# Optimization experiments

Hardware: AMD Instinct MI355X
Metric: run time of the kernel (lower is better)

## Reference

```python
import jax, jax.numpy as jnp
import numpy as np

ANG = 7
N = ANG * ANG          # 49 views
CENTER = N // 2        # index 24 = central view
EDGE_C = 150.0
ALPHA = 0.1
CROP = 8
GAUSS = jnp.array([[0.0751, 0.1238, 0.0751],
                   [0.1238, 0.2042, 0.1238],
                   [0.0751, 0.1238, 0.0751]], dtype=jnp.float32)


def _edge_aware_smoothness(D, I):
    # D: [b,h,w] disparity; I: [b,3,h,w] center view
    gx = I[:, :, :, 1:] - I[:, :, :, :-1]
    gy = I[:, :, 1:, :] - I[:, :, :-1, :]
    wx = jnp.exp(-EDGE_C * jnp.mean(jnp.abs(gx), axis=1, keepdims=True))
    wy = jnp.exp(-EDGE_C * jnp.mean(jnp.abs(gy), axis=1, keepdims=True))
    Du = D[:, None]
    dgx = Du[:, :, :, 1:] - Du[:, :, :, :-1]
    dgy = Du[:, :, 1:, :] - Du[:, :, :-1, :]
    lx = jnp.mean((wx * jnp.abs(dgx))[:, :, CROP:-CROP, CROP:-CROP])
    ly = jnp.mean((wy * jnp.abs(dgy))[:, :, CROP:-CROP, CROP:-CROP])
    return (lx + ly) / 2.0


def _warp_all(pred, x):
    # Backward-warp each of the 49 views toward the center view using the
    # per-pixel disparity scaled by the view's angular offset (bilinear,
    # border-clamped) -- standard light-field warping (warp_all in the repo).
    # pred: [b,h,w]; x: [b,3,N,h,w] -> warped [b,3,N,h,w]
    b, c, n, h, w = x.shape
    off = jnp.arange(ANG, dtype=pred.dtype) - (ANG // 2)
    du = jnp.repeat(off, ANG)   # row (u) offset per view, [N]
    dv = jnp.tile(off, ANG)     # col (v) offset per view, [N]
    gy = jnp.arange(h, dtype=pred.dtype)[:, None]
    gx = jnp.arange(w, dtype=pred.dtype)[None, :]
    p = pred[:, None, :, :]                                # [b,1,h,w]
    cy = jnp.clip(gy[None, None] + p * du[None, :, None, None], 0.0, h - 1)
    cx = jnp.clip(gx[None, None] + p * dv[None, :, None, None], 0.0, w - 1)
    y0f = jnp.floor(cy); x0f = jnp.floor(cx)
    ty = (cy - y0f)[..., None]; tx = (cx - x0f)[..., None]
    y0 = y0f.astype(jnp.int32); x0 = x0f.astype(jnp.int32)
    y1 = jnp.minimum(y0 + 1, h - 1); x1 = jnp.minimum(x0 + 1, w - 1)
    img = jnp.transpose(x, (0, 2, 3, 4, 1)).reshape(b, n, h * w, c)

    def gather(yi, xi):
        idx = (yi * w + xi).reshape(b, n, h * w, 1)
        return jnp.take_along_axis(img, idx, axis=2).reshape(b, n, h, w, c)

    out = (gather(y0, x0) * (1 - ty) * (1 - tx)
           + gather(y0, x1) * (1 - ty) * tx
           + gather(y1, x0) * ty * (1 - tx)
           + gather(y1, x1) * ty * tx)
    return jnp.transpose(out, (0, 4, 1, 2, 3))


def _gauss_smooth_angular(cl):
    # cl [b,1,N,h,w]: 3x3 gaussian conv over the 7x7 angular grid, replicate pad
    b, _, _, h, w = cl.shape
    g = cl.reshape(b, 1, ANG, ANG, h, w)
    g = jnp.pad(g, ((0, 0), (0, 0), (1, 1), (1, 1), (0, 0), (0, 0)), mode='edge')
    out = sum(GAUSS[i, j] * g[:, :, i:i + ANG, j:j + ANG]
              for i in range(3) for j in range(3))
    return out.reshape(b, 1, N, h, w)


def _forward(pred, x, y, epoch):
    b, u, v, h, w, c = x.shape
    # 'b u v h w c -> b c (u v) h w'
    xr = jnp.transpose(x, (0, 5, 1, 2, 3, 4)).reshape(b, c, N, h, w)
    center = xr[:, :, CENTER]                               # [b,3,h,w]
    grad_loss = _edge_aware_smoothness(pred, center)
    warped = _warp_all(pred, xr)                            # [b,3,N,h,w]
    color_loss = jnp.mean(jnp.abs(warped - warped[:, :, CENTER:CENTER + 1]),
                          axis=1, keepdims=True)            # [b,1,N,h,w]
    if epoch > 0:
        gauss = jax.lax.stop_gradient(_gauss_smooth_angular(color_loss))
        idx = jnp.argsort(-gauss, axis=2)                   # descending
        sorted_cl = jnp.take_along_axis(color_loss, idx, axis=2)
    else:
        sorted_cl = -jnp.sort(-color_loss, axis=2)
    yb = y[:, None, None, :, :]
    ar = jnp.arange(N, dtype=y.dtype)[None, None, :, None, None]
    mask = (ar > yb).astype(color_loss.dtype) / (N - yb) * N
    if epoch > 0:
        mask = jax.lax.stop_gradient(mask)                  # torch no_grad branch
    cl = jnp.mean((sorted_cl * mask)[..., CROP:-CROP, CROP:-CROP])
    return cl + grad_loss * ALPHA


def setup_inputs():
    key = jax.random.key(0)
    k1, k2, k3 = jax.random.split(key, 3)
    b, h, w = 4, 256, 256
    pred = jax.random.normal(k1, (b, h, w), dtype=jnp.float32)
    x = jax.random.uniform(k2, (b, ANG, ANG, h, w, 3), dtype=jnp.float32)
    y = jax.random.uniform(k3, (b, h, w), dtype=jnp.float32) * 24.0  # keep ~half views
    return {"pred": pred, "x": x, "y": y, "epoch": 5}


def reference(pred, x, y, epoch):
    return _forward(pred, x, y, epoch)
```

## Files before the change

### kernel.cpp

```cpp
#include <hip/hip_runtime.h>
#include <math.h>

#define NV    49
#define NVP   52
#define Himg  256
#define Wimg  256
#define RW    240
#define RWH   (RW*RW)
#define NPIX  (4*RWH)
#define ROWF  (Wimg*3)
#define IMGF  (Himg*Wimg*3)
#define NBLK  (NPIX/64)

typedef float f4u __attribute__((ext_vector_type(4), aligned(4)));
typedef float f2u __attribute__((ext_vector_type(2), aligned(4)));
typedef float f4a __attribute__((ext_vector_type(4), aligned(16)));


__global__ __launch_bounds__(448, 4) void color_kernel(
    const float* __restrict__ pred, const float* __restrict__ x,
    const float* __restrict__ y, const int* __restrict__ epoch_p,
    double* __restrict__ acc)
{
    __shared__ float s_cl[64 * NVP];
    __shared__ float s_g [64 * NVP];
    __shared__ float sred[8];

    const int tid = threadIdx.x;
    const int pix = tid & 63;
    const int sub = __builtin_amdgcn_readfirstlane(tid >> 6);

    int lb  = (blockIdx.x & 7) * (NBLK/8) + (blockIdx.x >> 3);
    int pid = lb * 64 + pix;
    int b   = pid / RWH;
    int rem = pid - b * RWH;
    int ry  = rem / RW;
    int yy  = 8 + ry;
    int xx  = 8 + (rem - ry * RW);

    int pidx = (b * Himg + yy) * Wimg + xx;
    float p    = pred[pidx];
    float yval = y[pidx];
    const int epoch = *epoch_p;

    const float* xv    = x + (size_t)b * (49 * IMGF);
    const float* cbase = xv + (24 * IMGF) + (yy * Wimg + xx) * 3;
    f4u cv = *(const f4u*)cbase;
    float c0 = cv.x, c1 = cv.y, c2 = cv.z;

    float* mycl = s_cl + pix * NVP;
    float* myg  = s_g  + pix * NVP;

    int co[7]; float txv[7];
    #pragma unroll
    for (int vv = 0; vv < 7; vv++) {
        float cx = fminf(fmaxf((float)xx + p * (float)(vv-3), 0.0f), 255.0f);
        float x0f = floorf(cx);
        float tx = cx - x0f;
        int ix0 = (int)x0f;
        if (ix0 >= 255) { ix0 = 254; tx = 1.0f; }
        co[vv] = ix0 * 3; txv[vv] = tx;
    }

    float creg[7];
    {
        float cy = fminf(fmaxf((float)yy + p * (float)(sub-3), 0.0f), 255.0f);
        float y0f = floorf(cy);
        float ty = cy - y0f;
        int iy0 = (int)y0f;
        int iy1 = min(iy0+1, 255);
        int ro0 = iy0*ROWF, ro1 = iy1*ROWF;
        const float* vbase = xv + sub * 7 * IMGF;

        f4u a0[4], b0[4]; f2u a1[4], b1[4];

#define LOADV(VV, S) { \
        const float* s0p = vbase + (VV)*IMGF + ro0 + co[VV]; \
        const float* s1p = vbase + (VV)*IMGF + ro1 + co[VV]; \
        a0[S] = *(const f4u*)s0p;  a1[S] = *(const f2u*)(s0p + 4); \
        b0[S] = *(const f4u*)s1p;  b1[S] = *(const f2u*)(s1p + 4); }

        LOADV(0,0) LOADV(1,1) LOADV(2,2)
        __builtin_amdgcn_sched_barrier(0);

        #pragma unroll
        for (int vv = 0; vv < 7; vv++) {
            if (vv + 3 < 7) { LOADV(vv+3, (vv+3)&3) }
            __builtin_amdgcn_sched_barrier(0);
            const int S = vv & 3;
            float tx = txv[vv];
            float s00 = a0[S].x, s01 = a0[S].y, s02 = a0[S].z;
            float s03 = a0[S].w, s04 = a1[S].x, s05 = a1[S].y;
            float s10 = b0[S].x, s11 = b0[S].y, s12 = b0[S].z;
            float s13 = b0[S].w, s14 = b1[S].x, s15 = b1[S].y;
            float h0 = s00 + tx*(s03-s00);
            float h1 = s01 + tx*(s04-s01);
            float h2 = s02 + tx*(s05-s02);
            float k0 = s10 + tx*(s13-s10);
            float k1 = s11 + tx*(s14-s11);
            float k2 = s12 + tx*(s15-s12);
            float o0 = h0 + ty*(k0-h0);
            float o1 = h1 + ty*(k1-h1);
            float o2 = h2 + ty*(k2-h2);
            float cl = (fabsf(o0-c0)+fabsf(o1-c1)+fabsf(o2-c2)) * (1.0f/3.0f);
            creg[vv] = cl;
            mycl[sub*7 + vv] = cl;
            __builtin_amdgcn_sched_barrier(0);
        }
#undef LOADV
    }

    if (sub == 3) {
        float lx = 0.0f, ly = 0.0f;
        if (xx <= 246) {
            f4u q0 = *(const f4u*)cbase;
            f2u q1 = *(const f2u*)(cbase + 4);
            float wx = __expf(-50.0f * (fabsf(q0.w-c0) + fabsf(q1.x-c1) + fabsf(q1.y-c2)));
            lx = wx * fabsf(pred[pidx + 1] - p);
        }
        if (yy <= 246) {
            f4u r = *(const f4u*)(cbase + ROWF);
            float wy = __expf(-50.0f * (fabsf(r.x-c0) + fabsf(r.y-c1) + fabsf(r.z-c2)));
            ly = wy * fabsf(pred[pidx + Wimg] - p);
        }
        #pragma unroll
        for (int off = 32; off > 0; off >>= 1) {
            lx += __shfl_down(lx, off);
            ly += __shfl_down(ly, off);
        }
        if (pix == 0) {
            atomicAdd(acc + 1, (double)lx);
            atomicAdd(acc + 2, (double)ly);
        }
    }
    __syncthreads();

    if (epoch > 0) {
        const int um1 = (sub > 0) ? sub-1 : 0;
        const int up1 = (sub < 6) ? sub+1 : 6;
        const float* rm = mycl + um1*7;
        const float* rc = mycl + sub*7;
        const float* rp = mycl + up1*7;
        #pragma unroll
        for (int vv = 0; vv < 7; vv++) {
            const int vm = (vv > 0) ? vv-1 : 0;
            const int vp = (vv < 6) ? vv+1 : 6;
            myg[sub*7 + vv] =
                0.0751f*rm[vm] + 0.1238f*rm[vv] + 0.0751f*rm[vp] +
                0.1238f*rc[vm] + 0.2042f*rc[vv] + 0.1238f*rc[vp] +
                0.0751f*rp[vm] + 0.1238f*rp[vv] + 0.0751f*rp[vp];
        }
    }
    __syncthreads();

    const float* keyb = (epoch > 0) ? myg : mycl;

    f4a kv[13];
    #pragma unroll
    for (int i = 0; i < 13; i++)
        kv[i] = *(const f4a*)(keyb + 4*i);

    unsigned long long kn[7];
    int cnt[7];
    #pragma unroll
    for (int i = 0; i < 7; i++) {
        int n = sub*7 + i;
        unsigned int bb = __float_as_uint(keyb[n]);
        kn[i] = (((unsigned long long)bb) << 8) | (unsigned long long)(255 - n);
        cnt[i] = 0;
    }
    #pragma unroll
    for (int m = 0; m < NV; m++) {
        unsigned int bm = __float_as_uint(kv[m>>2][m&3]);
        unsigned long long km = (((unsigned long long)bm) << 8) | (unsigned long long)(255 - m);
        #pragma unroll
        for (int i = 0; i < 7; i++)
            cnt[i] += (km > kn[i]) ? 1 : 0;
    }
    float tail = 0.0f;
    #pragma unroll
    for (int i = 0; i < 7; i++)
        tail += ((float)cnt[i] > yval) ? creg[i] : 0.0f;
    float contrib = tail * (49.0f / (49.0f - yval));

    #pragma unroll
    for (int off = 32; off > 0; off >>= 1)
        contrib += __shfl_down(contrib, off);
    if (pix == 0) sred[sub] = contrib;
    __syncthreads();
    if (tid == 0) {
        double s = 0.0;
        #pragma unroll
        for (int i = 0; i < 7; i++) s += (double)sred[i];
        atomicAdd(acc + 0, s);
    }
}

__global__ void finalize_kernel(const double* __restrict__ acc,
                                float* __restrict__ out)
{
    double cl = acc[0] / 11289600.0;
    double gl = (acc[1] + acc[2]) / (2.0 * 229440.0);
    out[0] = (float)(cl + 0.1 * gl);
}

extern "C" void kernel_launch(void* const* d_in, const int* in_sizes, int n_in,
                              void* d_out, int out_size, void* d_ws, size_t ws_size,
                              hipStream_t stream)
{
    const float* pred  = (const float*)d_in[0];
    const float* x     = (const float*)d_in[1];
    const float* y     = (const float*)d_in[2];
    const int*   epoch = (const int*)d_in[3];
    double* acc = (double*)d_ws;

    hipMemsetAsync(acc, 0, 3 * sizeof(double), stream);
    color_kernel<<<NBLK, 448, 0, stream>>>(pred, x, y, epoch, acc);
    finalize_kernel<<<1, 1, 0, stream>>>(acc, (float*)d_out);
}
```

Baseline: 320.3 us.

## Split fused color kernel into per-view cl kernel and per-pixel rank kernel

Replaces the single fused kernel with two passes. The first computes the per-view color loss with one thread per pixel and view, plus the smoothness term, and writes it to a workspace buffer. The second loads all 49 values per pixel into registers, does the angular Gaussian smoothing and rank counting, and accumulates the result. This removes the shared-memory exchange and the sync stalls, and gives a more regular gather pattern per view. In exchange it adds about 45 MB of intermediate writes and reads and heavy register pressure in the rank kernel. The old kernel is kept as a fallback when the workspace is too small.

New measurement: 497.9 us. +55.4%, slower.

```diff
diff --git a/kernel.cpp b/kernel.cpp
--- a/kernel.cpp
+++ b/kernel.cpp
@@ -15,6 +15,152 @@
 typedef float f4u __attribute__((ext_vector_type(4), aligned(4)));
 typedef float f2u __attribute__((ext_vector_type(2), aligned(4)));
 typedef float f4a __attribute__((ext_vector_type(4), aligned(16)));
+
+
+__global__ __launch_bounds__(256) void cl_kernel(
+    const float* __restrict__ pred, const float* __restrict__ x,
+    float* __restrict__ clbuf, double* __restrict__ acc)
+{
+    const int tid = threadIdx.x;
+    const int nb  = blockIdx.y;
+    const int b   = nb & 3;
+    const int n   = nb >> 2;
+    const int u   = n / 7, v = n - u*7;
+
+    int pix = blockIdx.x*256 + tid;
+    int ry  = pix / RW;
+    int rx  = pix - ry*RW;
+    int yy  = 8 + ry, xx = 8 + rx;
+    int pidx = (b*Himg + yy)*Wimg + xx;
+    float p = pred[pidx];
+
+    const float* xv    = x + (size_t)b * (49*IMGF);
+    const float* cbase = xv + 24*IMGF + (yy*Wimg+xx)*3;
+    f4u cv = *(const f4u*)cbase;
+    float c0 = cv.x, c1 = cv.y, c2 = cv.z;
+
+    float cx  = fminf(fmaxf((float)xx + p*(float)(v-3), 0.0f), 255.0f);
+    float x0f = floorf(cx);
+    float tx  = cx - x0f;
+    int ix0   = (int)x0f;
+    if (ix0 >= 255) { ix0 = 254; tx = 1.0f; }
+    float cy  = fminf(fmaxf((float)yy + p*(float)(u-3), 0.0f), 255.0f);
+    float y0f = floorf(cy);
+    float ty  = cy - y0f;
+    int iy0   = (int)y0f;
+    int iy1   = min(iy0+1, 255);
+
+    const float* ib  = xv + n*IMGF;
+    const float* s0p = ib + iy0*ROWF + ix0*3;
+    const float* s1p = ib + iy1*ROWF + ix0*3;
+    f4u a0 = *(const f4u*)s0p;  f2u a1 = *(const f2u*)(s0p + 4);
+    f4u b0 = *(const f4u*)s1p;  f2u b1 = *(const f2u*)(s1p + 4);
+
+    float s00 = a0.x, s01 = a0.y, s02 = a0.z;
+    float s03 = a0.w, s04 = a1.x, s05 = a1.y;
+    float s10 = b0.x, s11 = b0.y, s12 = b0.z;
+    float s13 = b0.w, s14 = b1.x, s15 = b1.y;
+    float h0 = s00 + tx*(s03-s00);
+    float h1 = s01 + tx*(s04-s01);
+    float h2 = s02 + tx*(s05-s02);
+    float k0 = s10 + tx*(s13-s10);
+    float k1 = s11 + tx*(s14-s11);
+    float k2 = s12 + tx*(s15-s12);
+    float o0 = h0 + ty*(k0-h0);
+    float o1 = h1 + ty*(k1-h1);
+    float o2 = h2 + ty*(k2-h2);
+    float cl = (fabsf(o0-c0)+fabsf(o1-c1)+fabsf(o2-c2)) * (1.0f/3.0f);
+
+    clbuf[(size_t)nb*RWH + pix] = cl;
+
+    if (n == 24) {
+        float lx = 0.0f, ly = 0.0f;
+        if (xx <= 246) {
+            f2u q1 = *(const f2u*)(cbase + 4);
+            float wx = __expf(-50.0f * (fabsf(cv.w-c0) + fabsf(q1.x-c1) + fabsf(q1.y-c2)));
+            lx = wx * fabsf(pred[pidx + 1] - p);
+        }
+        if (yy <= 246) {
+            f4u r = *(const f4u*)(cbase + ROWF);
+            float wy = __expf(-50.0f * (fabsf(r.x-c0) + fabsf(r.y-c1) + fabsf(r.z-c2)));
+            ly = wy * fabsf(pred[pidx + Wimg] - p);
+        }
+        #pragma unroll
+        for (int off = 32; off > 0; off >>= 1) {
+            lx += __shfl_down(lx, off);
+            ly += __shfl_down(ly, off);
+        }
+        if ((tid & 63) == 0) {
+            atomicAdd(acc + 1, (double)lx);
+            atomicAdd(acc + 2, (double)ly);
+        }
+    }
+}
+
+
+__global__ __launch_bounds__(256) void rank_kernel(
+    const float* __restrict__ clbuf, const float* __restrict__ y,
+    const int* __restrict__ epoch_p, double* __restrict__ acc)
+{
+    __shared__ float sred[4];
+    const int tid  = threadIdx.x;
+    int gpix = blockIdx.x*256 + tid;
+    int b    = gpix / RWH;
+    int pix  = gpix - b*RWH;
+    int ry   = pix / RW, rx = pix - ry*RW;
+    int yy   = 8 + ry,   xx = 8 + rx;
+    float yval = y[(b*Himg + yy)*Wimg + xx];
+    const int epoch = *epoch_p;
+
+    float cl[49];
+    #pragma unroll
+    for (int n = 0; n < 49; n++)
+        cl[n] = clbuf[(size_t)n*NPIX + gpix];
+
+    float g[49];
+    if (epoch > 0) {
+        #pragma unroll
+        for (int u = 0; u < 7; u++) {
+            const int um1 = (u > 0) ? u-1 : 0;
+            const int up1 = (u < 6) ? u+1 : 6;
+            #pragma unroll
+            for (int v = 0; v < 7; v++) {
+                const int vm = (v > 0) ? v-1 : 0;
+                const int vp = (v < 6) ? v+1 : 6;
+                g[u*7+v] =
+                    0.0751f*cl[um1*7+vm] + 0.1238f*cl[um1*7+v] + 0.0751f*cl[um1*7+vp] +
+                    0.1238f*cl[u*7+vm]   + 0.2042f*cl[u*7+v]   + 0.1238f*cl[u*7+vp] +
+                    0.0751f*cl[up1*7+vm] + 0.1238f*cl[up1*7+v] + 0.0751f*cl[up1*7+vp];
+            }
+        }
+    } else {
+        #pragma unroll
+        for (int n = 0; n < 49; n++) g[n] = cl[n];
+    }
+
+    float tail = 0.0f;
+    #pragma unroll
+    for (int n = 0; n < 49; n++) {
+        unsigned int bn = __float_as_uint(g[n]);
+        int cnt = 0;
+        #pragma unroll
+        for (int m = 0; m < 49; m++) {
+            if (m == n) continue;
+            unsigned int bm = __float_as_uint(g[m]);
+            cnt += ((m < n) ? (bm >= bn) : (bm > bn)) ? 1 : 0;
+        }
+        tail += ((float)cnt > yval) ? cl[n] : 0.0f;
+    }
+    float contrib = tail * (49.0f / (49.0f - yval));
+
+    #pragma unroll
+    for (int off = 32; off > 0; off >>= 1)
+        contrib += __shfl_down(contrib, off);
+    if ((tid & 63) == 0) sred[tid >> 6] = contrib;
+    __syncthreads();
+    if (tid == 0)
+        atomicAdd(acc + 0, (double)(sred[0] + sred[1] + sred[2] + sred[3]));
+}
 
 
 __global__ __launch_bounds__(448, 4) void color_kernel(
@@ -212,9 +358,18 @@
     const float* x     = (const float*)d_in[1];
     const float* y     = (const float*)d_in[2];
     const int*   epoch = (const int*)d_in[3];
-    double* acc = (double*)d_ws;
+    double* acc  = (double*)d_ws;
 
     hipMemsetAsync(acc, 0, 3 * sizeof(double), stream);
-    color_kernel<<<NBLK, 448, 0, stream>>>(pred, x, y, epoch, acc);
+
+    const size_t need = 256 + (size_t)NV * NPIX * sizeof(float);
+    if (ws_size >= need) {
+        float* clbuf = (float*)((char*)d_ws + 256);
+        dim3 ga(RWH/256, 196);
+        cl_kernel<<<ga, 256, 0, stream>>>(pred, x, clbuf, acc);
+        rank_kernel<<<NPIX/256, 256, 0, stream>>>(clbuf, y, epoch, acc);
+    } else {
+        color_kernel<<<NBLK, 448, 0, stream>>>(pred, x, y, epoch, acc);
+    }
     finalize_kernel<<<1, 1, 0, stream>>>(acc, (float*)d_out);
 }
```
